# Performance work log

Hardware: AMD Instinct MI355X
Metric: run time of the kernel (lower is better)

Reference implementation:

```python
import jax, jax.numpy as jnp
import numpy as np

H_GRID = 256
W_GRID = 256


def setup_inputs() -> dict:
    key = jax.random.key(0)
    k1, k2, k3, k4 = jax.random.split(key, 4)
    B, N = 8, 32768
    in_ch, out_ch = 14, 64
    xyzp = jax.random.uniform(k1, (B, N, 4), dtype=jnp.float32)  # x,y,t,p all in [0,1]
    features = jax.random.normal(k2, (B, N, in_ch), dtype=jnp.float32)
    W = jax.random.normal(k3, (9, in_ch + 2, out_ch), dtype=jnp.float32) * 0.05  # 3x3 kernel taps
    bias = jax.random.normal(k4, (out_ch,), dtype=jnp.float32) * 0.05
    return {"xyzp": xyzp, "features": features, "W": W, "bias": bias}


def reference(xyzp, features, W, bias):
    # SparseConv: voxelize points onto an (h+1)x(w+1) grid with 'mean' pooling of
    # duplicates, run a 3x3 submanifold sparse conv (inactive sites contribute 0),
    # then map results back to point order.
    h, w = H_GRID, W_GRID
    Hd, Wd = h + 1, w + 1  # round(y*h) in [0,h]
    B, N, _ = xyzp.shape
    Cin = features.shape[-1] + 2

    # yxb coordinates (note: column order [y, x] as in _get_yxb)
    y = jnp.clip(jnp.round(xyzp[..., 1] * h), 0, h).astype(jnp.int32).reshape(-1)
    x = jnp.clip(jnp.round(xyzp[..., 0] * w), 0, w).astype(jnp.int32).reshape(-1)
    b = jnp.repeat(jnp.arange(B, dtype=jnp.int32), N)

    # per-point features: [pos, neg, features]
    p = xyzp[..., 3:4]
    f = jnp.concatenate([p, 1.0 - p, features], axis=-1).reshape(B * N, Cin)

    # InputLayer mode='mean': scatter-mean duplicate coordinates into voxels
    flat = (b * Hd + y) * Wd + x  # [B*N]
    S = B * Hd * Wd
    vox_sum = jax.ops.segment_sum(f, flat, num_segments=S)            # [S, Cin]
    cnt = jax.ops.segment_sum(jnp.ones((B * N, 1), f.dtype), flat, num_segments=S)
    vox = vox_sum / jnp.maximum(cnt, 1.0)  # inactive voxels stay exactly 0

    # Submanifold 3x3 conv evaluated at each point's (active) site.
    offs = jnp.array([(dy, dx) for dy in (-1, 0, 1) for dx in (-1, 0, 1)], jnp.int32)  # [9,2]
    ny = y[:, None] + offs[None, :, 0]  # [B*N, 9]
    nx = x[:, None] + offs[None, :, 1]
    valid = (ny >= 0) & (ny < Hd) & (nx >= 0) & (nx < Wd)
    nidx = (b[:, None] * Hd + jnp.clip(ny, 0, Hd - 1)) * Wd + jnp.clip(nx, 0, Wd - 1)
    nb = vox[nidx] * valid[..., None].astype(f.dtype)  # [B*N, 9, Cin]; inactive -> 0

    out = jnp.einsum('pkc,kcd->pd', nb, W) + bias  # [B*N, out_ch]
    return out.reshape(B, N, -1)
```

## Files before the change

kernel.cpp:

```cpp
#include <hip/hip_runtime.h>

#define HD 257
#define WD 257
#define NB (8 * HD)
#define NCHUNK 32
#define CAPC 32
#define BPTS 1024
#define COUT 64
#define LROW 17
#define RPB 2
#define GPTS 64

typedef unsigned int uint;
typedef unsigned short ushort;
typedef short short8 __attribute__((ext_vector_type(8)));
typedef float f32x4 __attribute__((ext_vector_type(4)));

__device__ __forceinline__ uint pack_bf16(float a, float b) {
    uint ua = __float_as_uint(a), ub = __float_as_uint(b);
    ua += 0x7fffu + ((ua >> 16) & 1u);
    ub += 0x7fffu + ((ub >> 16) & 1u);
    return (ua >> 16) | (ub & 0xffff0000u);
}

__global__ void wprep_kernel(const float* __restrict__ W, uint4* __restrict__ Wb) {
    int idx = blockIdx.x * blockDim.x + threadIdx.x;
    if (idx >= 5 * 4 * 64) return;
    int s = idx >> 8;
    int hi = (idx >> 6) & 3;
    int col = idx & 63;
    uint o[4];
#pragma unroll
    for (int jj = 0; jj < 4; ++jj) {
        int k0 = s * 32 + hi * 8 + 2 * jj;
        float fl = (k0 < 144) ? W[(size_t)k0 * 64 + col] : 0.0f;
        float fh = (k0 + 1 < 144) ? W[(size_t)(k0 + 1) * 64 + col] : 0.0f;
        o[jj] = pack_bf16(fl, fh);
    }
    Wb[idx] = make_uint4(o[0], o[1], o[2], o[3]);
}

__global__ __launch_bounds__(256) void bin_kernel(
    const float* __restrict__ xyzp,
    uint* __restrict__ cnt2,
    ushort* __restrict__ pidx,
    int N) {
    __shared__ uint hist[HD];
    const int tid = threadIdx.x;
    const int chunk = blockIdx.x;
    const int b = blockIdx.y;
    const int p0 = chunk * BPTS;
    for (int i = tid; i < HD; i += 256) hist[i] = 0u;
    __syncthreads();

    const float4* xp = reinterpret_cast<const float4*>(xyzp) + (size_t)b * N;
    uint rec[BPTS / 256];
#pragma unroll
    for (int k = 0; k < BPTS / 256; ++k) {
        int i = p0 + tid + k * 256;
        float4 v = xp[i];
        int y = (int)fminf(fmaxf(rintf(v.y * 256.0f), 0.0f), 256.0f);
        uint r = atomicAdd(&hist[y], 1u);
        rec[k] = (uint)y | (r << 9);
    }
    __syncthreads();

    for (int y = tid; y < HD; y += 256)
        cnt2[(size_t)(b * HD + y) * NCHUNK + chunk] = min(hist[y], (uint)CAPC);

#pragma unroll
    for (int k = 0; k < BPTS / 256; ++k) {
        int y = rec[k] & 511;
        uint r = rec[k] >> 9;
        if (r < CAPC)
            pidx[((size_t)(b * HD + y) * NCHUNK + chunk) * CAPC + r] =
                (ushort)(p0 + tid + k * 256);
    }
}

__global__ __launch_bounds__(256) void accum_kernel(
    const uint* __restrict__ cnt2,
    const ushort* __restrict__ pidx,
    const float* __restrict__ xyzp,
    const float* __restrict__ feat,
    uint* __restrict__ voxn,
    int logN) {
    __shared__ float l[RPB * WD * LROW];
    __shared__ uint pc[RPB * NCHUNK];
    const int tid = threadIdx.x;
    const int bucket0 = blockIdx.x * RPB;
    for (int i = tid; i < RPB * WD * LROW; i += 256) l[i] = 0.0f;
    if (tid < RPB * NCHUNK)
        pc[tid] = cnt2[(size_t)bucket0 * NCHUNK + tid];
    __syncthreads();

    for (uint s = tid; ; s += 256) {
        uint c = 0, acc = 0;
        while (c < RPB * NCHUNK) {
            uint h = pc[c];
            if (s < acc + h) break;
            acc += h;
            ++c;
        }
        if (c == RPB * NCHUNK) break;
        uint j = s - acc;
        int r = (int)(c >> 5);
        int chunk = (int)(c & 31);
        int bucket = bucket0 + r;
        int b = bucket / HD;
        uint lp = pidx[((size_t)bucket * NCHUNK + chunk) * CAPC + j];
        int p = (b << logN) + (int)lp;
        float4 v = reinterpret_cast<const float4*>(xyzp)[p];
        int x = (int)fminf(fmaxf(rintf(v.x * 256.0f), 0.0f), 256.0f);
        float* cell = l + (r * WD + x) * LROW;
        atomicAdd(&cell[0], v.w);
        atomicAdd(&cell[1], 1.0f - v.w);
        const float2* f2 = reinterpret_cast<const float2*>(feat + (size_t)p * 14);
#pragma unroll
        for (int jj = 0; jj < 7; ++jj) {
            float2 fv = f2[jj];
            atomicAdd(&cell[2 + 2 * jj], fv.x);
            atomicAdd(&cell[3 + 2 * jj], fv.y);
        }
    }
    __syncthreads();

    for (int i = tid; i < RPB * WD; i += 256) {
        int r = i / WD;
        int x = i - r * WD;
        const float* c = l + (r * WD + x) * LROW;
        float inv = __builtin_amdgcn_rcpf(fmaxf(c[0] + c[1], 1.0f));
        uint o[8];
#pragma unroll
        for (int j = 0; j < 8; ++j)
            o[j] = pack_bf16(c[2 * j] * inv, c[2 * j + 1] * inv);
        uint4* op = reinterpret_cast<uint4*>(voxn + ((size_t)(bucket0 + r) * WD + x) * 8);
        op[0] = make_uint4(o[0], o[1], o[2], o[3]);
        op[1] = make_uint4(o[4], o[5], o[6], o[7]);
    }
}

__global__ __launch_bounds__(256) void gather_mfma_kernel(
    const float* __restrict__ xyzp,
    const uint* __restrict__ voxn,
    const uint4* __restrict__ Wb,
    const float* __restrict__ bias,
    float* __restrict__ out, int logN) {
    __shared__ __align__(16) char sA[GPTS * 336];
    __shared__ int sCell[GPTS];
    __shared__ uint sYX[GPTS];

    const int tid = threadIdx.x;
    const int lane = tid & 63;
    const int w = tid >> 6;
    const int p0 = blockIdx.x * GPTS;
    const int hi = lane >> 4;
    const int lo = lane & 15;

    if (tid < GPTS) {
        float4 v = reinterpret_cast<const float4*>(xyzp)[p0 + tid];
        int y = (int)fminf(fmaxf(rintf(v.y * 256.0f), 0.0f), 256.0f);
        int x = (int)fminf(fmaxf(rintf(v.x * 256.0f), 0.0f), 256.0f);
        int b = (p0 + tid) >> logN;
        sCell[tid] = (b * HD + y) * WD + x;
        sYX[tid] = ((uint)y << 16) | (uint)x;
    }

    short8 bfrag[5];
    float bv = bias[w * 16 + lo];
    {
        const uint4* wb = Wb + hi * 64 + (w * 16 + lo);
#pragma unroll
        for (int s = 0; s < 5; ++s)
            bfrag[s] = *reinterpret_cast<const short8*>(&wb[(size_t)s * 256]);
    }
    __syncthreads();

    for (int idx = tid; idx < GPTS * 18; idx += 256) {
        int i = idx / 18;
        int r = idx - i * 18;
        int seg = r / 6;
        int h = r - seg * 6;
        int kx = h >> 1;
        int half = h & 1;
        uint yx = sYX[i];
        int y = (int)(yx >> 16), x = (int)(yx & 0xffffu);
        int ny = y + seg - 1, nx = x + kx - 1;
        uint4 val = make_uint4(0, 0, 0, 0);
        if ((uint)ny <= 256u && (uint)nx <= 256u) {
            size_t ncell = (size_t)sCell[i] + (size_t)((seg - 1) * WD + (kx - 1));
            val = *reinterpret_cast<const uint4*>(
                reinterpret_cast<const char*>(voxn) + ncell * 32 + (size_t)half * 16);
        }
        *reinterpret_cast<uint4*>(sA + i * 336 + (seg * 3 + kx) * 32 + half * 16) = val;
    }
    if (tid < GPTS * 2) {
        int i = tid >> 1, h = tid & 1;
        *reinterpret_cast<uint4*>(sA + i * 336 + 288 + h * 16) = make_uint4(0, 0, 0, 0);
    }
    __syncthreads();

    f32x4 acc[4];
#pragma unroll
    for (int mt = 0; mt < 4; ++mt) acc[mt] = (f32x4){bv, bv, bv, bv};

#pragma unroll
    for (int mt = 0; mt < 4; ++mt) {
        const char* abase = sA + (mt * 16 + lo) * 336 + hi * 16;
#pragma unroll
        for (int s = 0; s < 5; ++s) {
            short8 a = *reinterpret_cast<const short8*>(abase + s * 64);
            acc[mt] = __builtin_amdgcn_mfma_f32_16x16x32_bf16(a, bfrag[s], acc[mt], 0, 0, 0);
        }
    }

#pragma unroll
    for (int mt = 0; mt < 4; ++mt)
#pragma unroll
        for (int r = 0; r < 4; ++r) {
            int row = mt * 16 + hi * 4 + r;
            out[(size_t)(p0 + row) * 64 + w * 16 + lo] = acc[mt][r];
        }
}

extern "C" void kernel_launch(void* const* d_in, const int* in_sizes, int n_in,
                              void* d_out, int out_size, void* d_ws, size_t ws_size,
                              hipStream_t stream) {
    const float* xyzp = (const float*)d_in[0];
    const float* feat = (const float*)d_in[1];
    const float* W    = (const float*)d_in[2];
    const float* bias = (const float*)d_in[3];
    float* out = (float*)d_out;

    const int BN = in_sizes[0] / 4;
    const int B = 8;
    const int N = BN / B;
    int logN = 0;
    while ((1 << logN) < N) ++logN;

    uint4* Wb = (uint4*)d_ws;
    uint* cnt2 = (uint*)((char*)d_ws + 5 * 4 * 64 * 16);
    ushort* pidx = (ushort*)((char*)cnt2 + (size_t)NB * NCHUNK * 4);
    uint* voxn = (uint*)((char*)pidx + (size_t)NB * NCHUNK * CAPC * 2);
    (void)ws_size;

    wprep_kernel<<<5, 256, 0, stream>>>(W, Wb);
    dim3 bgrid(NCHUNK, B);
    bin_kernel<<<bgrid, 256, 0, stream>>>(xyzp, cnt2, pidx, N);
    accum_kernel<<<NB / RPB, 256, 0, stream>>>(cnt2, pidx, xyzp, feat, voxn, logN);
    gather_mfma_kernel<<<BN / GPTS, 256, 0, stream>>>(xyzp, voxn, Wb, bias, out, logN);
}
```

Before: 79.35 us.

## Fold weight prep into gather kernel and use fixed slot loop in accumulation

The separate weight-prep kernel launch is removed. Each gather block now loads the fp32 weights itself and converts them to bf16 MFMA fragments, which saves one launch at the cost of redundant strided weight loads in every block. The accumulation kernel no longer does a per-thread prefix scan over chunk counts to find its work item. Instead it walks a fixed grid of capacity slots and skips empty ones, which wastes lanes on empty slots but drops the serial search loop.

```diff
diff --git a/kernel.cpp b/kernel.cpp
--- a/kernel.cpp
+++ b/kernel.cpp
@@ -22,22 +22,10 @@
     ub += 0x7fffu + ((ub >> 16) & 1u);
     return (ua >> 16) | (ub & 0xffff0000u);
 }
-
-__global__ void wprep_kernel(const float* __restrict__ W, uint4* __restrict__ Wb) {
-    int idx = blockIdx.x * blockDim.x + threadIdx.x;
-    if (idx >= 5 * 4 * 64) return;
-    int s = idx >> 8;
-    int hi = (idx >> 6) & 3;
-    int col = idx & 63;
-    uint o[4];
-#pragma unroll
-    for (int jj = 0; jj < 4; ++jj) {
-        int k0 = s * 32 + hi * 8 + 2 * jj;
-        float fl = (k0 < 144) ? W[(size_t)k0 * 64 + col] : 0.0f;
-        float fh = (k0 + 1 < 144) ? W[(size_t)(k0 + 1) * 64 + col] : 0.0f;
-        o[jj] = pack_bf16(fl, fh);
-    }
-    Wb[idx] = make_uint4(o[0], o[1], o[2], o[3]);
+__device__ __forceinline__ unsigned short bf16_1(float a) {
+    uint ua = __float_as_uint(a);
+    ua += 0x7fffu + ((ua >> 16) & 1u);
+    return (unsigned short)(ua >> 16);
 }
 
 __global__ __launch_bounds__(256) void bin_kernel(
@@ -94,33 +82,30 @@
         pc[tid] = cnt2[(size_t)bucket0 * NCHUNK + tid];
     __syncthreads();
 
-    for (uint s = tid; ; s += 256) {
-        uint c = 0, acc = 0;
-        while (c < RPB * NCHUNK) {
-            uint h = pc[c];
-            if (s < acc + h) break;
-            acc += h;
-            ++c;
-        }
-        if (c == RPB * NCHUNK) break;
-        uint j = s - acc;
-        int r = (int)(c >> 5);
-        int chunk = (int)(c & 31);
-        int bucket = bucket0 + r;
-        int b = bucket / HD;
-        uint lp = pidx[((size_t)bucket * NCHUNK + chunk) * CAPC + j];
-        int p = (b << logN) + (int)lp;
-        float4 v = reinterpret_cast<const float4*>(xyzp)[p];
-        int x = (int)fminf(fmaxf(rintf(v.x * 256.0f), 0.0f), 256.0f);
-        float* cell = l + (r * WD + x) * LROW;
-        atomicAdd(&cell[0], v.w);
-        atomicAdd(&cell[1], 1.0f - v.w);
-        const float2* f2 = reinterpret_cast<const float2*>(feat + (size_t)p * 14);
-#pragma unroll
-        for (int jj = 0; jj < 7; ++jj) {
-            float2 fv = f2[jj];
-            atomicAdd(&cell[2 + 2 * jj], fv.x);
-            atomicAdd(&cell[3 + 2 * jj], fv.y);
+#pragma unroll
+    for (int s = 0; s < RPB * NCHUNK * CAPC; s += 256) {
+        int slot = s + tid;
+        int c = slot >> 5;
+        int j = slot & (CAPC - 1);
+        if ((uint)j < pc[c]) {
+            int r = c >> 5;
+            int chunk = c & 31;
+            int bucket = bucket0 + r;
+            int b = bucket / HD;
+            uint lp = pidx[((size_t)bucket * NCHUNK + chunk) * CAPC + j];
+            int p = (b << logN) + (int)lp;
+            float4 v = reinterpret_cast<const float4*>(xyzp)[p];
+            int x = (int)fminf(fmaxf(rintf(v.x * 256.0f), 0.0f), 256.0f);
+            float* cell = l + (r * WD + x) * LROW;
+            atomicAdd(&cell[0], v.w);
+            atomicAdd(&cell[1], 1.0f - v.w);
+            const float2* f2 = reinterpret_cast<const float2*>(feat + (size_t)p * 14);
+#pragma unroll
+            for (int jj = 0; jj < 7; ++jj) {
+                float2 fv = f2[jj];
+                atomicAdd(&cell[2 + 2 * jj], fv.x);
+                atomicAdd(&cell[3 + 2 * jj], fv.y);
+            }
         }
     }
     __syncthreads();
@@ -143,7 +128,7 @@
 __global__ __launch_bounds__(256) void gather_mfma_kernel(
     const float* __restrict__ xyzp,
     const uint* __restrict__ voxn,
-    const uint4* __restrict__ Wb,
+    const float* __restrict__ W,
     const float* __restrict__ bias,
     float* __restrict__ out, int logN) {
     __shared__ __align__(16) char sA[GPTS * 336];
@@ -168,11 +153,17 @@
 
     short8 bfrag[5];
     float bv = bias[w * 16 + lo];
-    {
-        const uint4* wb = Wb + hi * 64 + (w * 16 + lo);
-#pragma unroll
-        for (int s = 0; s < 5; ++s)
-            bfrag[s] = *reinterpret_cast<const short8*>(&wb[(size_t)s * 256]);
+#pragma unroll
+    for (int s = 0; s < 5; ++s) {
+        int kbase = s * 32 + hi * 8;
+        short8 f;
+#pragma unroll
+        for (int j = 0; j < 8; ++j) {
+            int k = kbase + j;
+            float wv = (k < 144) ? W[(size_t)k * 64 + w * 16 + lo] : 0.0f;
+            f[j] = (short)bf16_1(wv);
+        }
+        bfrag[s] = f;
     }
     __syncthreads();
 
@@ -238,15 +229,13 @@
     int logN = 0;
     while ((1 << logN) < N) ++logN;
 
-    uint4* Wb = (uint4*)d_ws;
-    uint* cnt2 = (uint*)((char*)d_ws + 5 * 4 * 64 * 16);
+    uint* cnt2 = (uint*)d_ws;
     ushort* pidx = (ushort*)((char*)cnt2 + (size_t)NB * NCHUNK * 4);
     uint* voxn = (uint*)((char*)pidx + (size_t)NB * NCHUNK * CAPC * 2);
     (void)ws_size;
 
-    wprep_kernel<<<5, 256, 0, stream>>>(W, Wb);
     dim3 bgrid(NCHUNK, B);
     bin_kernel<<<bgrid, 256, 0, stream>>>(xyzp, cnt2, pidx, N);
     accum_kernel<<<NB / RPB, 256, 0, stream>>>(cnt2, pidx, xyzp, feat, voxn, logN);
-    gather_mfma_kernel<<<BN / GPTS, 256, 0, stream>>>(xyzp, voxn, Wb, bias, out, logN);
-}
+    gather_mfma_kernel<<<BN / GPTS, 256, 0, stream>>>(xyzp, voxn, W, bias, out, logN);
+}
```

After: 70.35 us. -11.3%, faster.
